# Kernel tuning notes

Measured on AMD Instinct MI355X. Metric: run time of the kernel, lower is better.

## Reference

```python
import jax, jax.numpy as jnp
import numpy as np
import math

Q_DIM = 1024
K_DIM = 1024
ATT_DIM = 1024
POS_DIM = 64
B, NQ, NK = 4, 2048, 2048
EPS = 1e-5


def _ln(x, g, b):
    m = jnp.mean(x, axis=-1, keepdims=True)
    v = jnp.var(x, axis=-1, keepdims=True)
    return (x - m) * jax.lax.rsqrt(v + EPS) * g + b


def _sinpos(n, dim):
    # SinPos: exp = 2*arange(dim//2)/dim; pos = p * 10000**-exp; cat(pos, pos+pi/2); sin
    e = 2.0 * jnp.arange(dim // 2, dtype=jnp.float32) / dim      # [dim/2]
    p = jnp.arange(n, dtype=jnp.float32)[:, None]                # [n,1]
    ph = p * jnp.power(10000.0, -e)[None, :]                     # [n,dim/2]
    return jnp.sin(jnp.concatenate([ph, ph + math.pi / 2], axis=1))  # [n,dim]


def setup_inputs() -> dict:
    key = jax.random.key(0)
    ks = jax.random.split(key, 8)
    s = 0.02
    return {
        "q": jax.random.normal(ks[0], (B, NQ, Q_DIM), jnp.float32),
        "k": jax.random.normal(ks[1], (B, NK, K_DIM), jnp.float32),
        "Wq": jax.random.normal(ks[2], (Q_DIM, ATT_DIM), jnp.float32) * s,
        "bq": jnp.zeros((ATT_DIM,), jnp.float32),
        "Wk": jax.random.normal(ks[3], (K_DIM, ATT_DIM), jnp.float32) * s,
        "bk": jnp.zeros((ATT_DIM,), jnp.float32),
        "Wv": jax.random.normal(ks[4], (K_DIM, ATT_DIM), jnp.float32) * s,
        "bv": jnp.zeros((ATT_DIM,), jnp.float32),
        "gq": jnp.ones((ATT_DIM,), jnp.float32), "betaq": jnp.zeros((ATT_DIM,), jnp.float32),
        "gk": jnp.ones((ATT_DIM,), jnp.float32), "betak": jnp.zeros((ATT_DIM,), jnp.float32),
        "gv": jnp.ones((ATT_DIM,), jnp.float32), "betav": jnp.zeros((ATT_DIM,), jnp.float32),
        "Wp": jax.random.normal(ks[5], (POS_DIM, POS_DIM), jnp.float32) * s,
        "bp": jnp.zeros((POS_DIM,), jnp.float32),
    }


def reference(q, k, Wq, bq, Wk, bk, Wv, bv, gq, betaq, gk, betak, gv, betav, Wp, bp):
    qn = _ln(q @ Wq + bq, gq, betaq)          # [B,NQ,D]
    vn = _ln(k @ Wv + bv, gv, betav)          # [B,NK,D]
    kn = _ln(k @ Wk + bk, gk, betak)          # [B,NK,D]
    pos = _sinpos(NK, POS_DIM)                # [NK,P]

    # attention 1: Q=qn, K=kn, V=pos
    s1 = jnp.einsum('bnd,bjd->bnj', qn, kn) * (1.0 / math.sqrt(ATT_DIM))
    a1 = jax.nn.softmax(s1, axis=-1)          # [B,NQ,NK]
    x = jnp.einsum('bnj,jp->bnp', a1, pos)    # [B,NQ,P]

    # pos_net (Linear)
    x = x @ Wp + bp                           # [B,NQ,P]

    # attention 2: Q=x, K=pos, V=vn
    s2 = jnp.einsum('bnp,jp->bnj', x, pos) * (1.0 / math.sqrt(POS_DIM))
    a2 = jax.nn.softmax(s2, axis=-1)          # [B,NQ,NK]
    out = jnp.einsum('bnj,bjd->bnd', a2, vn)  # [B,NQ,D]

    att = jnp.stack([a1, a2], axis=1)         # [B,2,NQ,NK] == torch.cat over head dim
    return out, att
```

## Files before the change

### kernel.cpp

```cpp
#include <hip/hip_runtime.h>
#include <math.h>
#include <stdint.h>


typedef _Float16 f16;
typedef _Float16 f16x4 __attribute__((ext_vector_type(4)));
typedef _Float16 f16x8 __attribute__((ext_vector_type(8)));
typedef float f32x4 __attribute__((ext_vector_type(4)));

static constexpr int CB  = 4;
static constexpr int CNQ = 2048;
static constexpr int CNK = 2048;
static constexpr int CD  = 1024;
static constexpr int CP  = 64;

static __device__ __forceinline__ void async16(const f16* gp, f16* lp) {
  __builtin_amdgcn_global_load_lds(
      (const __attribute__((address_space(1))) void*)(uintptr_t)gp,
      (__attribute__((address_space(3))) void*)(uint32_t)(uintptr_t)lp,
      16, 0, 0);
}

__global__ __launch_bounds__(256) void prep_kernel(
    const float* __restrict__ q, const float* __restrict__ k,
    const float* __restrict__ Wq, const float* __restrict__ Wk,
    const float* __restrict__ Wv,
    f16* __restrict__ q16, f16* __restrict__ k16,
    f16* __restrict__ WqT, f16* __restrict__ WkvT,
    f16* __restrict__ posb, f16* __restrict__ posTb) {
  const int b = blockIdx.x;
  if (b < 512) {
    int tid = b * 256 + threadIdx.x;
    int p = tid >> 11;
    int j = tid & (CNK - 1);
    int i = p & 31;
    float ph = (float)j * powf(10000.0f, -(float)i * (1.0f / 32.0f));
    float v = (p < 32) ? sinf(ph) : cosf(ph);
    posb[j * CP + p]   = (f16)v;
    posTb[p * CNK + j] = (f16)v;
  } else if (b < 512 + 16384) {
    const int NF4 = CB * CNQ * CD / 4;
    int tid = (b - 512) * 256 + threadIdx.x;
    const float* src = (tid < NF4) ? q : k;
    f16* dst = (tid < NF4) ? q16 : k16;
    int i = (tid < NF4) ? tid : tid - NF4;
    float4 v = reinterpret_cast<const float4*>(src)[i];
    f16x4 o = {(f16)v.x, (f16)v.y, (f16)v.z, (f16)v.w};
    reinterpret_cast<f16x4*>(dst)[i] = o;
  } else {
    __shared__ float t[64][65];
    const int idx = b - 16896;
    const int z = idx >> 8;
    const int rem = idx & 255;
    const float* W = (z == 0) ? Wq : (z == 1) ? Wk : Wv;
    f16* WT = (z == 0) ? WqT : (z == 1) ? WkvT : WkvT + 1024 * 1024;
    int k0 = (rem & 15) * 64, n0 = (rem >> 4) * 64;
    int tx = threadIdx.x & 63, ty = threadIdx.x >> 6;
#pragma unroll
    for (int i = 0; i < 16; i++)
      t[ty + 4 * i][tx] = W[(size_t)(k0 + ty + 4 * i) * CD + n0 + tx];
    __syncthreads();
#pragma unroll
    for (int i = 0; i < 16; i++)
      WT[(size_t)(n0 + 4 * i + ty) * CD + k0 + tx] = (f16)t[tx][ty + 4 * i];
  }
}

__global__ __launch_bounds__(256) void transpose_kernel(const f16* __restrict__ in,
                                                        f16* __restrict__ out,
                                                        int ldi) {
  __shared__ f16 t[64][65];
  int n0 = blockIdx.x * 64, d0 = blockIdx.y * 64;
  size_t ibase = (size_t)blockIdx.z * CNK * ldi;
  size_t obase = (size_t)blockIdx.z * CNK * CD;
  int tx = threadIdx.x & 63, ty = threadIdx.x >> 6;
#pragma unroll
  for (int i = 0; i < 16; i++)
    t[ty + 4 * i][tx] = in[ibase + (size_t)(n0 + ty + 4 * i) * ldi + d0 + tx];
  __syncthreads();
#pragma unroll
  for (int i = 0; i < 16; i++)
    out[obase + (size_t)(d0 + ty + 4 * i) * CNK + n0 + tx] = t[tx][ty + 4 * i];
}

template <int BM, int BN>
__device__ __forceinline__ void gemm_core3(
    const f16* __restrict__ Ab, const f16* __restrict__ Bb,
    int lda, int ldb, int K, int m0, int n0, f16* sm,
    f32x4 (&acc)[BM / 32][BN / 64]) {
  constexpr int FM = BM / 32, FN = BN / 64;
  constexpr int TI = (BM + BN) / 64;
  constexpr int bufsz = (BM + BN) * 64;
  const int tid = threadIdx.x;
  const int lane = tid & 63, wid = tid >> 6;
  const int wr = wid >> 2, wc = wid & 3;
  const int lrow = lane & 15, kg = lane >> 4;

  auto stage = [&](int i, int kt, int buf) {
    const int s = i * 512 + tid;
    const int row = s >> 3;
    const int cb = (s & 7) << 4;
    const int scb = cb ^ ((row & 7) << 4);
    const f16* src = (i < BM / 64)
        ? Ab + (size_t)(m0 + row) * lda + kt * 64 + (scb >> 1)
        : Bb + (size_t)(n0 + row - BM) * ldb + kt * 64 + (scb >> 1);
    async16(src, &sm[buf * bufsz + s * 8]);
  };

  const int NT = K >> 6;
#pragma unroll
  for (int i = 0; i < TI; i++) stage(i, 0, 0);
#pragma unroll
  for (int i = 0; i < TI; i++) stage(i, 1, 1);

  for (int t = 0; t < NT; ++t) {
    if (t + 2 < NT) {
      const int b2 = (t + 2) % 3;
#pragma unroll
      for (int i = 0; i < TI; i++) stage(i, t + 2, b2);
      asm volatile("s_waitcnt vmcnt(12)" ::: "memory");
    } else if (t + 2 == NT) {
      asm volatile("s_waitcnt vmcnt(6)" ::: "memory");
    } else {
      asm volatile("s_waitcnt vmcnt(0)" ::: "memory");
    }
    __builtin_amdgcn_s_barrier();

    const f16* smA = sm + (t % 3) * bufsz;
    const f16* smB = smA + BM * 64;
#pragma unroll
    for (int kk = 0; kk < 2; ++kk) {
      const int Cb = kk * 64 + kg * 16;
      f16x8 af[FM], bf[FN];
#pragma unroll
      for (int m = 0; m < FM; ++m) {
        const int ar = wr * (BM / 2) + m * 16 + lrow;
        af[m] = *reinterpret_cast<const f16x8*>(
            &smA[ar * 64 + ((Cb ^ ((ar & 7) << 4)) >> 1)]);
      }
#pragma unroll
      for (int n = 0; n < FN; ++n) {
        const int br = wc * (BN / 4) + n * 16 + lrow;
        bf[n] = *reinterpret_cast<const f16x8*>(
            &smB[br * 64 + ((Cb ^ ((br & 7) << 4)) >> 1)]);
      }
      __builtin_amdgcn_s_barrier();
      __builtin_amdgcn_s_setprio(1);
#pragma unroll
      for (int m = 0; m < FM; ++m)
#pragma unroll
        for (int n = 0; n < FN; ++n)
          acc[m][n] = __builtin_amdgcn_mfma_f32_16x16x32_f16(af[m], bf[n], acc[m][n], 0, 0, 0);
      __builtin_amdgcn_s_setprio(0);
      __builtin_amdgcn_s_barrier();
    }
  }
}

template <int BM, int BN>
__device__ __forceinline__ void epi_f16(
    f32x4 (&acc)[BM / 32][BN / 64], f16* sm, f16* Cp, int ldc, int m0, int n0) {
  const int tid = threadIdx.x, lane = tid & 63, wid = tid >> 6;
  const int wr = wid >> 2, wc = wid & 3;
  const int rbase = wr * (BM / 2) + (lane >> 4) * 4;
  const int cbase = wc * (BN / 4) + (lane & 15);
  __syncthreads();
#pragma unroll
  for (int mg = 0; mg < BM / 32; mg++)
#pragma unroll
    for (int n = 0; n < BN / 64; n++)
#pragma unroll
      for (int r = 0; r < 4; r++)
        sm[(rbase + mg * 16 + r) * BN + cbase + n * 16] = (f16)acc[mg][n][r];
  __syncthreads();
  constexpr int CH = BM * BN / (512 * 8);
#pragma unroll
  for (int c = 0; c < CH; c++) {
    const int idx = c * 512 + tid;
    const int row = idx / (BN / 8);
    const int cole = (idx % (BN / 8)) * 8;
    f16x8 v = *reinterpret_cast<const f16x8*>(&sm[row * BN + cole]);
    *reinterpret_cast<f16x8*>(Cp + (size_t)(m0 + row) * ldc + n0 + cole) = v;
  }
}

template <int BM, int BN>
__device__ __forceinline__ void epi_exp(
    f32x4 (&acc)[BM / 32][BN / 64], f16* sm, float* psum, f16* Cp, int ldc,
    int m0, int n0, float scale, float* PSrow) {
  constexpr int SL = BN / 8;
  const int tid = threadIdx.x, lane = tid & 63, wid = tid >> 6;
  const int wr = wid >> 2, wc = wid & 3;
  const int rbase = wr * (BM / 2) + (lane >> 4) * 4;
  const int cbase = wc * (BN / 4) + (lane & 15);
  __syncthreads();
#pragma unroll
  for (int mg = 0; mg < BM / 32; mg++)
#pragma unroll
    for (int n = 0; n < BN / 64; n++)
#pragma unroll
      for (int r = 0; r < 4; r++)
        sm[(rbase + mg * 16 + r) * BN + cbase + n * 16] =
            (f16)__expf(acc[mg][n][r] * scale);
  __syncthreads();
  constexpr int CH = BM * BN / (512 * 8);
#pragma unroll
  for (int c = 0; c < CH; c++) {
    const int idx = c * 512 + tid;
    const int row = idx / SL;
    const int cole = (idx % SL) * 8;
    f16x8 v = *reinterpret_cast<const f16x8*>(&sm[row * BN + cole]);
    *reinterpret_cast<f16x8*>(Cp + (size_t)(m0 + row) * ldc + n0 + cole) = v;
    float p = 0.f;
#pragma unroll
    for (int j = 0; j < 8; j++) p += (float)v[j];
#pragma unroll
    for (int o = 1; o < SL; o <<= 1) p += __shfl_xor(p, o);
    if ((lane & (SL - 1)) == 0) psum[row] = p;
  }
  __syncthreads();
  if (tid < BM) PSrow[tid] = psum[tid];
}

template <int BM, int BN>
__device__ __forceinline__ void epi_f32(
    f32x4 (&acc)[BM / 32][BN / 64], f16* smh, float* Cp, int ldc, int m0, int n0) {
  float* st = (float*)smh;
  const int tid = threadIdx.x, lane = tid & 63, wid = tid >> 6;
  const int wr = wid >> 2, wc = wid & 3;
  const int cbase = wc * (BN / 4) + (lane & 15);
#pragma unroll
  for (int half = 0; half < 2; half++) {
    __syncthreads();
    if (wr == half) {
#pragma unroll
      for (int mg = 0; mg < BM / 32; mg++)
#pragma unroll
        for (int r = 0; r < 4; r++) {
          const int rloc = (lane >> 4) * 4 + mg * 16 + r;
#pragma unroll
          for (int n = 0; n < BN / 64; n++)
            st[rloc * BN + cbase + n * 16] = acc[mg][n][r];
        }
    }
    __syncthreads();
    constexpr int CH = (BM / 2) * BN / (512 * 4);
#pragma unroll
    for (int c = 0; c < CH; c++) {
      const int idx = c * 512 + tid;
      const int row = idx / (BN / 4);
      const int cole = (idx % (BN / 4)) * 4;
      float4 v = *reinterpret_cast<const float4*>(&st[row * BN + cole]);
      *reinterpret_cast<float4*>(
          Cp + (size_t)(m0 + half * (BM / 2) + row) * ldc + n0 + cole) = v;
    }
  }
}

__global__ __launch_bounds__(512) void gemmIn_kernel(
    const f16* __restrict__ q16, const f16* __restrict__ WqT, f16* __restrict__ tmpq,
    const f16* __restrict__ k16, const f16* __restrict__ WkvT, f16* __restrict__ tmp2) {
  __shared__ __attribute__((aligned(16))) f16 sm[3 * (256 + 128) * 64];
  const int b = blockIdx.x;
  const int swz = (b & 7) * 96 + (b >> 3);
  const f16 *A, *B;
  f16* C;
  int ldc, m0, n0;
  if (swz < 256) {
    const int by = swz >> 5, bx = swz & 31;
    A = q16; B = WqT; C = tmpq; ldc = 1024; m0 = bx * 256; n0 = by * 128;
  } else {
    const int idx = swz - 256;
    const int by = idx >> 5, bx = idx & 31;
    A = k16; B = WkvT; C = tmp2; ldc = 2048; m0 = bx * 256; n0 = by * 128;
  }
  f32x4 acc[8][2] = {};
  gemm_core3<256, 128>(A, B, 1024, 1024, 1024, m0, n0, sm, acc);
  epi_f16<256, 128>(acc, sm, C, ldc, m0, n0);
}

__global__ __launch_bounds__(512) void gemmS1_kernel(
    const f16* __restrict__ qn, const f16* __restrict__ kn,
    f16* __restrict__ e1, float* __restrict__ PS) {
  __shared__ __attribute__((aligned(16))) f16 sm[3 * (256 + 128) * 64];
  __shared__ float psum[256];
  const int b = blockIdx.x;
  const int swz = (b & 7) * 64 + (b >> 3);
  const int bz = swz >> 7;
  const int rem = swz & 127;
  const int by = rem >> 3, bx = rem & 7;
  const int m0 = bx * 256, n0 = by * 128;
  const f16* Ab = qn + (size_t)bz * 2048 * 1024;
  const f16* Bb = kn + (size_t)bz * 2048 * 2048;
  f16* Cp = e1 + (size_t)bz * 2048 * 2048;
  f32x4 acc[8][2] = {};
  gemm_core3<256, 128>(Ab, Bb, 1024, 2048, 1024, m0, n0, sm, acc);
  epi_exp<256, 128>(acc, sm, psum, Cp, 2048, m0, n0, 0.03125f,
                    PS + (size_t)by * 8192 + bz * 2048 + m0);
}

__global__ __launch_bounds__(512) void gemmOut_kernel(
    const f16* __restrict__ e2, const f16* __restrict__ vnT, float* __restrict__ out) {
  __shared__ __attribute__((aligned(16))) f16 sm[3 * (256 + 128) * 64];
  const int b = blockIdx.x;
  const int swz = (b & 7) * 32 + (b >> 3);
  const int bz = swz >> 6;
  const int rem = swz & 63;
  const int by = rem >> 3, bx = rem & 7;
  const int m0 = bx * 256, n0 = by * 128;
  const f16* Ab = e2 + (size_t)bz * 2048 * 2048;
  const f16* Bb = vnT + (size_t)bz * 1024 * 2048;
  float* Cp = out + (size_t)bz * 2048 * 1024;
  f32x4 acc[8][2] = {};
  gemm_core3<256, 128>(Ab, Bb, 2048, 2048, 2048, m0, n0, sm, acc);
  epi_f32<256, 128>(acc, sm, Cp, 1024, m0, n0);
}

__global__ __launch_bounds__(256) void ln3_kernel(
    f16* __restrict__ tmpq, f16* __restrict__ tmp2,
    const float* __restrict__ bq, const float* __restrict__ gq, const float* __restrict__ beq,
    const float* __restrict__ bk, const float* __restrict__ gk, const float* __restrict__ bek,
    const float* __restrict__ bv, const float* __restrict__ gv, const float* __restrict__ bev) {
  __shared__ float rs_[4], rq_[4];
  const int z = blockIdx.y;
  f16* rp;
  const float *bias, *g, *beta;
  if (z == 0)      { rp = tmpq + (size_t)blockIdx.x * 1024;        bias = bq; g = gq; beta = beq; }
  else if (z == 1) { rp = tmp2 + (size_t)blockIdx.x * 2048;        bias = bk; g = gk; beta = bek; }
  else             { rp = tmp2 + (size_t)blockIdx.x * 2048 + 1024; bias = bv; g = gv; beta = bev; }
  const int t = threadIdx.x;
  f16x4 v = *reinterpret_cast<const f16x4*>(rp + t * 4);
  float y[4], s = 0.f, q = 0.f;
#pragma unroll
  for (int j = 0; j < 4; j++) {
    y[j] = (float)v[j] + bias[t * 4 + j];
    s += y[j]; q += y[j] * y[j];
  }
#pragma unroll
  for (int o = 32; o; o >>= 1) { s += __shfl_xor(s, o); q += __shfl_xor(q, o); }
  if ((t & 63) == 0) { rs_[t >> 6] = s; rq_[t >> 6] = q; }
  __syncthreads();
  s = rs_[0] + rs_[1] + rs_[2] + rs_[3];
  q = rq_[0] + rq_[1] + rq_[2] + rq_[3];
  const float mean = s * (1.0f / CD);
  const float rstd = rsqrtf(q * (1.0f / CD) - mean * mean + 1e-5f);
  f16x4 o;
#pragma unroll
  for (int j = 0; j < 4; j++) {
    int c = t * 4 + j;
    o[j] = (f16)((y[j] - mean) * rstd * g[c] + beta[c]);
  }
  *reinterpret_cast<f16x4*>(rp + t * 4) = o;
}

__global__ __launch_bounds__(256) void xgemm_kernel(
    const f16* __restrict__ e1, const f16* __restrict__ posTb,
    const float* __restrict__ PS, float* __restrict__ xw, float* __restrict__ att) {
  constexpr int BM = 64, BN = 64;
  __shared__ __attribute__((aligned(16))) f16 As[BM * 32];
  __shared__ __attribute__((aligned(16))) f16 Bs[BN * 32];
  __shared__ float invs[BM];
  const int tid = threadIdx.x;
  const int lane = tid & 63;
  const int wave = tid >> 6;
  const int wr = wave >> 1, wc = wave & 1;
  const int m0 = blockIdx.x * BM;
  const int kbase = blockIdx.z * 1024;
  const int srow = lane >> 2;
  const int scol = (lane & 3) * 8;
  const int lrow = lane & 15;
  const int kg = lane >> 4;

  if (tid < BM) {
    float s = 0.f;
#pragma unroll
    for (int j = 0; j < 16; j++) s += PS[j * (CB * CNQ) + m0 + tid];
    invs[tid] = 1.0f / s;
  }

  const int bb = m0 >> 11, nloc = m0 & (CNQ - 1);
  float* attb = att + ((size_t)(bb << 1) * CNQ + nloc) * CNK + kbase;
  const int arow = tid >> 2, acol = (tid & 3) * 8;

  f32x4 acc[2][2] = {};
  for (int k0 = 0; k0 < 1024; k0 += 32) {
    __syncthreads();
#pragma unroll
    for (int i = wave; i < 8; i += 4) {
      if (i < 4)
        async16(e1 + (size_t)(m0 + i * 16 + srow) * CNK + kbase + k0 + scol, &As[i * 512]);
      else
        async16(posTb + (size_t)((i - 4) * 16 + srow) * CNK + kbase + k0 + scol,
                &Bs[(i - 4) * 512]);
    }
    __syncthreads();
    f16x8 af[2], bfr[2];
#pragma unroll
    for (int m = 0; m < 2; m++)
      af[m] = *reinterpret_cast<const f16x8*>(&As[(wr * 32 + m * 16 + lrow) * 32 + kg * 8]);
#pragma unroll
    for (int n = 0; n < 2; n++)
      bfr[n] = *reinterpret_cast<const f16x8*>(&Bs[(wc * 32 + n * 16 + lrow) * 32 + kg * 8]);
#pragma unroll
    for (int m = 0; m < 2; m++)
#pragma unroll
      for (int n = 0; n < 2; n++)
        acc[m][n] = __builtin_amdgcn_mfma_f32_16x16x32_f16(af[m], bfr[n], acc[m][n], 0, 0, 0);
    {
      const float iv = invs[arow];
      f16x8 v = *reinterpret_cast<const f16x8*>(&As[arow * 32 + acol]);
      float4 w0 = {(float)v[0] * iv, (float)v[1] * iv, (float)v[2] * iv, (float)v[3] * iv};
      float4 w1 = {(float)v[4] * iv, (float)v[5] * iv, (float)v[6] * iv, (float)v[7] * iv};
      float* ap = attb + (size_t)arow * CNK + k0 + acol;
      reinterpret_cast<float4*>(ap)[0] = w0;
      reinterpret_cast<float4*>(ap)[1] = w1;
    }
  }
  float* Cp = xw + (size_t)blockIdx.z * (CB * CNQ) * CP;
  const int crow = m0 + wr * 32 + (lane >> 4) * 4;
  const int ccol = wc * 32 + (lane & 15);
#pragma unroll
  for (int m = 0; m < 2; m++)
#pragma unroll
    for (int n = 0; n < 2; n++)
#pragma unroll
      for (int r = 0; r < 4; r++)
        Cp[(size_t)(crow + m * 16 + r) * CP + ccol + n * 16] = acc[m][n][r];
}

__global__ __launch_bounds__(128) void attn2_kernel(
    const float* __restrict__ xw, const float* __restrict__ Wp,
    const float* __restrict__ bp, const f16* __restrict__ posb,
    const float* __restrict__ PS, f16* __restrict__ e2,
    float* __restrict__ att) {
  __shared__ __attribute__((aligned(16))) f16 shm[32 * 2048 + 32 * 64];
  __shared__ float rsum[32];
  __shared__ float invs[32];
  f16* e2lds = shm;
  f16* xpb = shm + 32 * 2048;
  float* xs = (float*)shm;
  float* Wps = (float*)shm + 32 * 64;
  const int tid = threadIdx.x, l = tid & 63, w = tid >> 6;
  const int r0 = blockIdx.x * 32;
  if (tid < 32) {
    float s = 0.f;
#pragma unroll
    for (int j = 0; j < 16; j++) s += PS[j * (CB * CNQ) + r0 + tid];
    invs[tid] = 1.0f / s;
  }
  __syncthreads();
#pragma unroll
  for (int i = 0; i < 16; i++) {
    const int row = w * 16 + i;
    const size_t gi = (size_t)(r0 + row) * CP + l;
    xs[row * 64 + l] = (xw[gi] + xw[(size_t)(CB * CNQ) * CP + gi]) * invs[row];
  }
#pragma unroll
  for (int i = w; i < 64; i += 2) Wps[i * 64 + l] = Wp[i * 64 + l];
  const float bpl = bp[l];
  __syncthreads();
  const int rb = w * 16;
#pragma unroll 2
  for (int i = 0; i < 16; i++) {
    float a = bpl;
#pragma unroll 8
    for (int p = 0; p < 64; p++) a = fmaf(xs[(rb + i) * 64 + p], Wps[p * 64 + l], a);
    xpb[(rb + i) * 64 + l] = (f16)a;
  }
  __syncthreads();
  const f16x8 af0 = *reinterpret_cast<const f16x8*>(&xpb[(rb + (l & 15)) * 64 + (l >> 4) * 8]);
  const f16x8 af1 = *reinterpret_cast<const f16x8*>(&xpb[(rb + (l & 15)) * 64 + 32 + (l >> 4) * 8]);
  float rs[4] = {0.f, 0.f, 0.f, 0.f};
  for (int jt = 0; jt < CNK / 64; jt++) {
#pragma unroll
    for (int q4 = 0; q4 < 4; q4++) {
      const int j = jt * 64 + q4 * 16 + (l & 15);
      const f16* pp = posb + (size_t)j * CP + (l >> 4) * 8;
      f16x8 b0 = *reinterpret_cast<const f16x8*>(pp);
      f16x8 b1 = *reinterpret_cast<const f16x8*>(pp + 32);
      f32x4 c = {};
      c = __builtin_amdgcn_mfma_f32_16x16x32_f16(af0, b0, c, 0, 0, 0);
      c = __builtin_amdgcn_mfma_f32_16x16x32_f16(af1, b1, c, 0, 0, 0);
#pragma unroll
      for (int r = 0; r < 4; r++) {
        float ev = __expf(c[r] * 0.125f);
        rs[r] += ev;
        e2lds[(rb + (l >> 4) * 4 + r) * 2048 + j] = (f16)ev;
      }
    }
  }
#pragma unroll
  for (int r = 0; r < 4; r++) {
#pragma unroll
    for (int o = 1; o < 16; o <<= 1) rs[r] += __shfl_xor(rs[r], o);
    if ((l & 15) == 0) rsum[rb + (l >> 4) * 4 + r] = rs[r];
  }
  __syncthreads();
  const int b = r0 >> 11, nloc = r0 & (CNQ - 1);
  float* attb = att + ((size_t)((b << 1) + 1) * CNQ + nloc) * CNK;
  f16* e2b = e2 + (size_t)r0 * CNK;
  for (int row = 0; row < 32; row++) {
    const float iv = 1.0f / rsum[row];
    const f16x8 a0 = *reinterpret_cast<const f16x8*>(&e2lds[row * 2048 + tid * 16]);
    const f16x8 a1 = *reinterpret_cast<const f16x8*>(&e2lds[row * 2048 + tid * 16 + 8]);
    float4 w0 = {(float)a0[0] * iv, (float)a0[1] * iv, (float)a0[2] * iv, (float)a0[3] * iv};
    float4 w1 = {(float)a0[4] * iv, (float)a0[5] * iv, (float)a0[6] * iv, (float)a0[7] * iv};
    float4 w2 = {(float)a1[0] * iv, (float)a1[1] * iv, (float)a1[2] * iv, (float)a1[3] * iv};
    float4 w3 = {(float)a1[4] * iv, (float)a1[5] * iv, (float)a1[6] * iv, (float)a1[7] * iv};
    float* ap = attb + (size_t)row * CNK + tid * 16;
    reinterpret_cast<float4*>(ap)[0] = w0;
    reinterpret_cast<float4*>(ap)[1] = w1;
    reinterpret_cast<float4*>(ap)[2] = w2;
    reinterpret_cast<float4*>(ap)[3] = w3;
    f16x8 h0 = {(f16)w0.x, (f16)w0.y, (f16)w0.z, (f16)w0.w,
                (f16)w1.x, (f16)w1.y, (f16)w1.z, (f16)w1.w};
    f16x8 h1 = {(f16)w2.x, (f16)w2.y, (f16)w2.z, (f16)w2.w,
                (f16)w3.x, (f16)w3.y, (f16)w3.z, (f16)w3.w};
    f16* ep = e2b + (size_t)row * CNK + tid * 16;
    *reinterpret_cast<f16x8*>(ep)     = h0;
    *reinterpret_cast<f16x8*>(ep + 8) = h1;
  }
}

extern "C" void kernel_launch(void* const* d_in, const int* in_sizes, int n_in,
                              void* d_out, int out_size, void* d_ws, size_t ws_size,
                              hipStream_t stream) {
  (void)in_sizes; (void)n_in; (void)out_size; (void)ws_size;
  const float* q    = (const float*)d_in[0];
  const float* k    = (const float*)d_in[1];
  const float* Wq   = (const float*)d_in[2];
  const float* bq   = (const float*)d_in[3];
  const float* Wk   = (const float*)d_in[4];
  const float* bk   = (const float*)d_in[5];
  const float* Wv   = (const float*)d_in[6];
  const float* bv   = (const float*)d_in[7];
  const float* gq   = (const float*)d_in[8];
  const float* betaq= (const float*)d_in[9];
  const float* gk   = (const float*)d_in[10];
  const float* betak= (const float*)d_in[11];
  const float* gv   = (const float*)d_in[12];
  const float* betav= (const float*)d_in[13];
  const float* Wp   = (const float*)d_in[14];
  const float* bp   = (const float*)d_in[15];

  float* out = (float*)d_out;
  float* att = out + (size_t)CB * CNQ * CD;
  char* ws = (char*)d_ws;
  const size_t MB = 1ull << 20;

  f16* q16   = (f16*)(ws);
  f16* k16   = (f16*)(ws + 16 * MB);
  f16* e1    = (f16*)(ws);
  f16* e2    = (f16*)(ws);
  f16* WqT   = (f16*)(ws + 32 * MB);
  f16* WkvT  = (f16*)(ws + 34 * MB);
  f16* posb  = (f16*)(ws + 38 * MB);
  f16* posTb = (f16*)(ws + 38 * MB + 256 * 1024);
  float* xw  = (float*)(ws + 38 * MB + 512 * 1024);
  float* PS  = (float*)(ws + 42 * MB + 512 * 1024);
  f16* tmpq  = (f16*)(ws + 43 * MB);
  f16* tmp2  = (f16*)(ws + 59 * MB);
  f16* vnT   = (f16*)(ws + 91 * MB);
  f16* qn = tmpq;
  f16* kn = tmp2;
  f16* vn = tmp2 + 1024;

  prep_kernel<<<512 + 16384 + 768, 256, 0, stream>>>(
      q, k, Wq, Wk, Wv, q16, k16, WqT, WkvT, posb, posTb);

  gemmIn_kernel<<<768, 512, 0, stream>>>(q16, WqT, tmpq, k16, WkvT, tmp2);
  ln3_kernel<<<dim3(CB * CNQ, 3), 256, 0, stream>>>(
      tmpq, tmp2, bq, gq, betaq, bk, gk, betak, bv, gv, betav);
  transpose_kernel<<<dim3(CNK / 64, CD / 64, CB), 256, 0, stream>>>(vn, vnT, 2048);

  gemmS1_kernel<<<512, 512, 0, stream>>>(qn, kn, e1, PS);

  xgemm_kernel<<<dim3(CB * CNQ / 64, 1, 2), 256, 0, stream>>>(e1, posTb, PS, xw, att);
  attn2_kernel<<<CB * CNQ / 32, 128, 0, stream>>>(xw, Wp, bp, posb, PS, e2, att);

  gemmOut_kernel<<<256, 512, 0, stream>>>(e2, vnT, out);
}
```

Before: 323.7 us.

## Retile GEMMs to double-buffered 128x256/256x256 tiles and widen attn2 blocks

```diff
diff --git a/kernel.cpp b/kernel.cpp
--- a/kernel.cpp
+++ b/kernel.cpp
@@ -84,11 +84,12 @@
 }
 
 template <int BM, int BN>
-__device__ __forceinline__ void gemm_core3(
+__device__ __forceinline__ void gemm_core(
     const f16* __restrict__ Ab, const f16* __restrict__ Bb,
     int lda, int ldb, int K, int m0, int n0, f16* sm,
-    f32x4 (&acc)[BM / 32][BN / 64]) {
-  constexpr int FM = BM / 32, FN = BN / 64;
+    f32x4 (&acc)[BM / 32][4]) {
+  constexpr int FM = BM / 32;
+  constexpr int FMC = FM / 2;
   constexpr int TI = (BM + BN) / 64;
   constexpr int bufsz = (BM + BN) * 64;
   const int tid = threadIdx.x;
@@ -107,50 +108,52 @@
     async16(src, &sm[buf * bufsz + s * 8]);
   };
 
-  const int NT = K >> 6;
+  const int NTk = K >> 6;
 #pragma unroll
   for (int i = 0; i < TI; i++) stage(i, 0, 0);
-#pragma unroll
-  for (int i = 0; i < TI; i++) stage(i, 1, 1);
-
-  for (int t = 0; t < NT; ++t) {
-    if (t + 2 < NT) {
-      const int b2 = (t + 2) % 3;
-#pragma unroll
-      for (int i = 0; i < TI; i++) stage(i, t + 2, b2);
-      asm volatile("s_waitcnt vmcnt(12)" ::: "memory");
-    } else if (t + 2 == NT) {
-      asm volatile("s_waitcnt vmcnt(6)" ::: "memory");
+
+  for (int t = 0; t < NTk; ++t) {
+    const int cur = t & 1;
+    if (t + 1 < NTk) {
+#pragma unroll
+      for (int i = 0; i < TI; i++) stage(i, t + 1, cur ^ 1);
+      if constexpr (TI == 8) asm volatile("s_waitcnt vmcnt(8)" ::: "memory");
+      else                   asm volatile("s_waitcnt vmcnt(6)" ::: "memory");
     } else {
       asm volatile("s_waitcnt vmcnt(0)" ::: "memory");
     }
     __builtin_amdgcn_s_barrier();
 
-    const f16* smA = sm + (t % 3) * bufsz;
+    const f16* smA = sm + cur * bufsz;
     const f16* smB = smA + BM * 64;
-#pragma unroll
-    for (int kk = 0; kk < 2; ++kk) {
+    f16x8 bf[2][4];
+#pragma unroll
+    for (int p = 0; p < 4; ++p) {
+      const int kk = p >> 1, mh = p & 1;
       const int Cb = kk * 64 + kg * 16;
-      f16x8 af[FM], bf[FN];
-#pragma unroll
-      for (int m = 0; m < FM; ++m) {
-        const int ar = wr * (BM / 2) + m * 16 + lrow;
+      f16x8 af[FMC];
+#pragma unroll
+      for (int m = 0; m < FMC; ++m) {
+        const int ar = wr * (BM / 2) + mh * (FMC * 16) + m * 16 + lrow;
         af[m] = *reinterpret_cast<const f16x8*>(
             &smA[ar * 64 + ((Cb ^ ((ar & 7) << 4)) >> 1)]);
       }
-#pragma unroll
-      for (int n = 0; n < FN; ++n) {
-        const int br = wc * (BN / 4) + n * 16 + lrow;
-        bf[n] = *reinterpret_cast<const f16x8*>(
-            &smB[br * 64 + ((Cb ^ ((br & 7) << 4)) >> 1)]);
+      if (mh == 0) {
+#pragma unroll
+        for (int n = 0; n < 4; ++n) {
+          const int br = wc * 64 + n * 16 + lrow;
+          bf[kk][n] = *reinterpret_cast<const f16x8*>(
+              &smB[br * 64 + ((Cb ^ ((br & 7) << 4)) >> 1)]);
+        }
       }
       __builtin_amdgcn_s_barrier();
       __builtin_amdgcn_s_setprio(1);
 #pragma unroll
-      for (int m = 0; m < FM; ++m)
-#pragma unroll
-        for (int n = 0; n < FN; ++n)
-          acc[m][n] = __builtin_amdgcn_mfma_f32_16x16x32_f16(af[m], bf[n], acc[m][n], 0, 0, 0);
+      for (int m = 0; m < FMC; ++m)
+#pragma unroll
+        for (int n = 0; n < 4; ++n)
+          acc[mh * FMC + m][n] = __builtin_amdgcn_mfma_f32_16x16x32_f16(
+              af[m], bf[kk][n], acc[mh * FMC + m][n], 0, 0, 0);
       __builtin_amdgcn_s_setprio(0);
       __builtin_amdgcn_s_barrier();
     }
@@ -159,16 +162,16 @@
 
 template <int BM, int BN>
 __device__ __forceinline__ void epi_f16(
-    f32x4 (&acc)[BM / 32][BN / 64], f16* sm, f16* Cp, int ldc, int m0, int n0) {
+    f32x4 (&acc)[BM / 32][4], f16* sm, f16* Cp, int ldc, int m0, int n0) {
   const int tid = threadIdx.x, lane = tid & 63, wid = tid >> 6;
   const int wr = wid >> 2, wc = wid & 3;
   const int rbase = wr * (BM / 2) + (lane >> 4) * 4;
-  const int cbase = wc * (BN / 4) + (lane & 15);
+  const int cbase = wc * 64 + (lane & 15);
   __syncthreads();
 #pragma unroll
   for (int mg = 0; mg < BM / 32; mg++)
 #pragma unroll
-    for (int n = 0; n < BN / 64; n++)
+    for (int n = 0; n < 4; n++)
 #pragma unroll
       for (int r = 0; r < 4; r++)
         sm[(rbase + mg * 16 + r) * BN + cbase + n * 16] = (f16)acc[mg][n][r];
@@ -186,18 +189,18 @@
 
 template <int BM, int BN>
 __device__ __forceinline__ void epi_exp(
-    f32x4 (&acc)[BM / 32][BN / 64], f16* sm, float* psum, f16* Cp, int ldc,
+    f32x4 (&acc)[BM / 32][4], f16* sm, float* psum, f16* Cp, int ldc,
     int m0, int n0, float scale, float* PSrow) {
   constexpr int SL = BN / 8;
   const int tid = threadIdx.x, lane = tid & 63, wid = tid >> 6;
   const int wr = wid >> 2, wc = wid & 3;
   const int rbase = wr * (BM / 2) + (lane >> 4) * 4;
-  const int cbase = wc * (BN / 4) + (lane & 15);
+  const int cbase = wc * 64 + (lane & 15);
   __syncthreads();
 #pragma unroll
   for (int mg = 0; mg < BM / 32; mg++)
 #pragma unroll
-    for (int n = 0; n < BN / 64; n++)
+    for (int n = 0; n < 4; n++)
 #pragma unroll
       for (int r = 0; r < 4; r++)
         sm[(rbase + mg * 16 + r) * BN + cbase + n * 16] =
@@ -224,11 +227,11 @@
 
 template <int BM, int BN>
 __device__ __forceinline__ void epi_f32(
-    f32x4 (&acc)[BM / 32][BN / 64], f16* smh, float* Cp, int ldc, int m0, int n0) {
+    f32x4 (&acc)[BM / 32][4], f16* smh, float* Cp, int ldc, int m0, int n0) {
   float* st = (float*)smh;
   const int tid = threadIdx.x, lane = tid & 63, wid = tid >> 6;
   const int wr = wid >> 2, wc = wid & 3;
-  const int cbase = wc * (BN / 4) + (lane & 15);
+  const int cbase = wc * 64 + (lane & 15);
 #pragma unroll
   for (int half = 0; half < 2; half++) {
     __syncthreads();
@@ -239,7 +242,7 @@
         for (int r = 0; r < 4; r++) {
           const int rloc = (lane >> 4) * 4 + mg * 16 + r;
 #pragma unroll
-          for (int n = 0; n < BN / 64; n++)
+          for (int n = 0; n < 4; n++)
             st[rloc * BN + cbase + n * 16] = acc[mg][n][r];
         }
     }
@@ -260,60 +263,60 @@
 __global__ __launch_bounds__(512) void gemmIn_kernel(
     const f16* __restrict__ q16, const f16* __restrict__ WqT, f16* __restrict__ tmpq,
     const f16* __restrict__ k16, const f16* __restrict__ WkvT, f16* __restrict__ tmp2) {
-  __shared__ __attribute__((aligned(16))) f16 sm[3 * (256 + 128) * 64];
+  __shared__ __attribute__((aligned(16))) f16 sm[2 * (128 + 256) * 64];
   const int b = blockIdx.x;
   const int swz = (b & 7) * 96 + (b >> 3);
   const f16 *A, *B;
   f16* C;
   int ldc, m0, n0;
   if (swz < 256) {
-    const int by = swz >> 5, bx = swz & 31;
-    A = q16; B = WqT; C = tmpq; ldc = 1024; m0 = bx * 256; n0 = by * 128;
+    const int bx = swz & 63, by = swz >> 6;
+    A = q16; B = WqT; C = tmpq; ldc = 1024; m0 = bx * 128; n0 = by * 256;
   } else {
     const int idx = swz - 256;
-    const int by = idx >> 5, bx = idx & 31;
-    A = k16; B = WkvT; C = tmp2; ldc = 2048; m0 = bx * 256; n0 = by * 128;
-  }
-  f32x4 acc[8][2] = {};
-  gemm_core3<256, 128>(A, B, 1024, 1024, 1024, m0, n0, sm, acc);
-  epi_f16<256, 128>(acc, sm, C, ldc, m0, n0);
+    const int bx = idx & 63, by = idx >> 6;
+    A = k16; B = WkvT; C = tmp2; ldc = 2048; m0 = bx * 128; n0 = by * 256;
+  }
+  f32x4 acc[4][4] = {};
+  gemm_core<128, 256>(A, B, 1024, 1024, 1024, m0, n0, sm, acc);
+  epi_f16<128, 256>(acc, sm, C, ldc, m0, n0);
 }
 
 __global__ __launch_bounds__(512) void gemmS1_kernel(
     const f16* __restrict__ qn, const f16* __restrict__ kn,
     f16* __restrict__ e1, float* __restrict__ PS) {
-  __shared__ __attribute__((aligned(16))) f16 sm[3 * (256 + 128) * 64];
+  __shared__ __attribute__((aligned(16))) f16 sm[2 * (256 + 256) * 64];
   __shared__ float psum[256];
-  const int b = blockIdx.x;
-  const int swz = (b & 7) * 64 + (b >> 3);
-  const int bz = swz >> 7;
-  const int rem = swz & 127;
-  const int by = rem >> 3, bx = rem & 7;
-  const int m0 = bx * 256, n0 = by * 128;
-  const f16* Ab = qn + (size_t)bz * 2048 * 1024;
-  const f16* Bb = kn + (size_t)bz * 2048 * 2048;
-  f16* Cp = e1 + (size_t)bz * 2048 * 2048;
-  f32x4 acc[8][2] = {};
-  gemm_core3<256, 128>(Ab, Bb, 1024, 2048, 1024, m0, n0, sm, acc);
-  epi_exp<256, 128>(acc, sm, psum, Cp, 2048, m0, n0, 0.03125f,
-                    PS + (size_t)by * 8192 + bz * 2048 + m0);
-}
-
-__global__ __launch_bounds__(512) void gemmOut_kernel(
-    const f16* __restrict__ e2, const f16* __restrict__ vnT, float* __restrict__ out) {
-  __shared__ __attribute__((aligned(16))) f16 sm[3 * (256 + 128) * 64];
   const int b = blockIdx.x;
   const int swz = (b & 7) * 32 + (b >> 3);
   const int bz = swz >> 6;
   const int rem = swz & 63;
-  const int by = rem >> 3, bx = rem & 7;
-  const int m0 = bx * 256, n0 = by * 128;
+  const int bx = rem & 7, by = rem >> 3;
+  const int m0 = bx * 256, n0 = by * 256;
+  const f16* Ab = qn + (size_t)bz * 2048 * 1024;
+  const f16* Bb = kn + (size_t)bz * 2048 * 2048;
+  f16* Cp = e1 + (size_t)bz * 2048 * 2048;
+  f32x4 acc[8][4] = {};
+  gemm_core<256, 256>(Ab, Bb, 1024, 2048, 1024, m0, n0, sm, acc);
+  epi_exp<256, 256>(acc, sm, psum, Cp, 2048, m0, n0, 0.03125f,
+                    PS + (size_t)by * (CB * CNQ) + bz * 2048 + m0);
+}
+
+__global__ __launch_bounds__(512) void gemmOut_kernel(
+    const f16* __restrict__ e2, const f16* __restrict__ vnT, float* __restrict__ out) {
+  __shared__ __attribute__((aligned(16))) f16 sm[2 * (128 + 256) * 64];
+  const int b = blockIdx.x;
+  const int swz = (b & 7) * 32 + (b >> 3);
+  const int bz = swz >> 6;
+  const int rem = swz & 63;
+  const int bx = rem & 15, by = rem >> 4;
+  const int m0 = bx * 128, n0 = by * 256;
   const f16* Ab = e2 + (size_t)bz * 2048 * 2048;
   const f16* Bb = vnT + (size_t)bz * 1024 * 2048;
   float* Cp = out + (size_t)bz * 2048 * 1024;
-  f32x4 acc[8][2] = {};
-  gemm_core3<256, 128>(Ab, Bb, 2048, 2048, 2048, m0, n0, sm, acc);
-  epi_f32<256, 128>(acc, sm, Cp, 1024, m0, n0);
+  f32x4 acc[4][4] = {};
+  gemm_core<128, 256>(Ab, Bb, 2048, 2048, 2048, m0, n0, sm, acc);
+  epi_f32<128, 256>(acc, sm, Cp, 1024, m0, n0);
 }
 
 __global__ __launch_bounds__(256) void ln3_kernel(
@@ -374,7 +377,7 @@
   if (tid < BM) {
     float s = 0.f;
 #pragma unroll
-    for (int j = 0; j < 16; j++) s += PS[j * (CB * CNQ) + m0 + tid];
+    for (int j = 0; j < 8; j++) s += PS[j * (CB * CNQ) + m0 + tid];
     invs[tid] = 1.0f / s;
   }
 
@@ -428,13 +431,13 @@
         Cp[(size_t)(crow + m * 16 + r) * CP + ccol + n * 16] = acc[m][n][r];
 }
 
-__global__ __launch_bounds__(128) void attn2_kernel(
+__global__ __launch_bounds__(256) void attn2_kernel(
     const float* __restrict__ xw, const float* __restrict__ Wp,
     const float* __restrict__ bp, const f16* __restrict__ posb,
     const float* __restrict__ PS, f16* __restrict__ e2,
     float* __restrict__ att) {
   __shared__ __attribute__((aligned(16))) f16 shm[32 * 2048 + 32 * 64];
-  __shared__ float rsum[32];
+  __shared__ float rsum2[2][32];
   __shared__ float invs[32];
   f16* e2lds = shm;
   f16* xpb = shm + 32 * 2048;
@@ -445,33 +448,37 @@
   if (tid < 32) {
     float s = 0.f;
 #pragma unroll
-    for (int j = 0; j < 16; j++) s += PS[j * (CB * CNQ) + r0 + tid];
+    for (int j = 0; j < 8; j++) s += PS[j * (CB * CNQ) + r0 + tid];
     invs[tid] = 1.0f / s;
   }
   __syncthreads();
-#pragma unroll
-  for (int i = 0; i < 16; i++) {
-    const int row = w * 16 + i;
-    const size_t gi = (size_t)(r0 + row) * CP + l;
-    xs[row * 64 + l] = (xw[gi] + xw[(size_t)(CB * CNQ) * CP + gi]) * invs[row];
-  }
-#pragma unroll
-  for (int i = w; i < 64; i += 2) Wps[i * 64 + l] = Wp[i * 64 + l];
+  if (w < 2) {
+#pragma unroll
+    for (int i = 0; i < 16; i++) {
+      const int row = w * 16 + i;
+      const size_t gi = (size_t)(r0 + row) * CP + l;
+      xs[row * 64 + l] = (xw[gi] + xw[(size_t)(CB * CNQ) * CP + gi]) * invs[row];
+    }
+#pragma unroll
+    for (int i = w; i < 64; i += 2) Wps[i * 64 + l] = Wp[i * 64 + l];
+  }
   const float bpl = bp[l];
   __syncthreads();
-  const int rb = w * 16;
+  const int rb = (w & 1) * 16, jh = w >> 1;
+  if (w < 2) {
 #pragma unroll 2
-  for (int i = 0; i < 16; i++) {
-    float a = bpl;
+    for (int i = 0; i < 16; i++) {
+      float a = bpl;
 #pragma unroll 8
-    for (int p = 0; p < 64; p++) a = fmaf(xs[(rb + i) * 64 + p], Wps[p * 64 + l], a);
-    xpb[(rb + i) * 64 + l] = (f16)a;
+      for (int p = 0; p < 64; p++) a = fmaf(xs[(w * 16 + i) * 64 + p], Wps[p * 64 + l], a);
+      xpb[(w * 16 + i) * 64 + l] = (f16)a;
+    }
   }
   __syncthreads();
   const f16x8 af0 = *reinterpret_cast<const f16x8*>(&xpb[(rb + (l & 15)) * 64 + (l >> 4) * 8]);
   const f16x8 af1 = *reinterpret_cast<const f16x8*>(&xpb[(rb + (l & 15)) * 64 + 32 + (l >> 4) * 8]);
   float rs[4] = {0.f, 0.f, 0.f, 0.f};
-  for (int jt = 0; jt < CNK / 64; jt++) {
+  for (int jt = jh * 16; jt < jh * 16 + 16; jt++) {
 #pragma unroll
     for (int q4 = 0; q4 < 4; q4++) {
       const int j = jt * 64 + q4 * 16 + (l & 15);
@@ -493,21 +500,23 @@
   for (int r = 0; r < 4; r++) {
 #pragma unroll
     for (int o = 1; o < 16; o <<= 1) rs[r] += __shfl_xor(rs[r], o);
-    if ((l & 15) == 0) rsum[rb + (l >> 4) * 4 + r] = rs[r];
+    if ((l & 15) == 0) rsum2[jh][rb + (l >> 4) * 4 + r] = rs[r];
   }
   __syncthreads();
   const int b = r0 >> 11, nloc = r0 & (CNQ - 1);
   float* attb = att + ((size_t)((b << 1) + 1) * CNQ + nloc) * CNK;
   f16* e2b = e2 + (size_t)r0 * CNK;
-  for (int row = 0; row < 32; row++) {
-    const float iv = 1.0f / rsum[row];
-    const f16x8 a0 = *reinterpret_cast<const f16x8*>(&e2lds[row * 2048 + tid * 16]);
-    const f16x8 a1 = *reinterpret_cast<const f16x8*>(&e2lds[row * 2048 + tid * 16 + 8]);
+  for (int it = 0; it < 16; it++) {
+    const int row = it * 2 + (tid >> 7);
+    const int col = (tid & 127) * 16;
+    const float iv = 1.0f / (rsum2[0][row] + rsum2[1][row]);
+    const f16x8 a0 = *reinterpret_cast<const f16x8*>(&e2lds[row * 2048 + col]);
+    const f16x8 a1 = *reinterpret_cast<const f16x8*>(&e2lds[row * 2048 + col + 8]);
     float4 w0 = {(float)a0[0] * iv, (float)a0[1] * iv, (float)a0[2] * iv, (float)a0[3] * iv};
     float4 w1 = {(float)a0[4] * iv, (float)a0[5] * iv, (float)a0[6] * iv, (float)a0[7] * iv};
     float4 w2 = {(float)a1[0] * iv, (float)a1[1] * iv, (float)a1[2] * iv, (float)a1[3] * iv};
     float4 w3 = {(float)a1[4] * iv, (float)a1[5] * iv, (float)a1[6] * iv, (float)a1[7] * iv};
-    float* ap = attb + (size_t)row * CNK + tid * 16;
+    float* ap = attb + (size_t)row * CNK + col;
     reinterpret_cast<float4*>(ap)[0] = w0;
     reinterpret_cast<float4*>(ap)[1] = w1;
     reinterpret_cast<float4*>(ap)[2] = w2;
@@ -516,7 +525,7 @@
                 (f16)w1.x, (f16)w1.y, (f16)w1.z, (f16)w1.w};
     f16x8 h1 = {(f16)w2.x, (f16)w2.y, (f16)w2.z, (f16)w2.w,
                 (f16)w3.x, (f16)w3.y, (f16)w3.z, (f16)w3.w};
-    f16* ep = e2b + (size_t)row * CNK + tid * 16;
+    f16* ep = e2b + (size_t)row * CNK + col;
     *reinterpret_cast<f16x8*>(ep)     = h0;
     *reinterpret_cast<f16x8*>(ep + 8) = h1;
   }
@@ -573,10 +582,10 @@
       tmpq, tmp2, bq, gq, betaq, bk, gk, betak, bv, gv, betav);
   transpose_kernel<<<dim3(CNK / 64, CD / 64, CB), 256, 0, stream>>>(vn, vnT, 2048);
 
-  gemmS1_kernel<<<512, 512, 0, stream>>>(qn, kn, e1, PS);
+  gemmS1_kernel<<<256, 512, 0, stream>>>(qn, kn, e1, PS);
 
   xgemm_kernel<<<dim3(CB * CNQ / 64, 1, 2), 256, 0, stream>>>(e1, posTb, PS, xw, att);
-  attn2_kernel<<<CB * CNQ / 32, 128, 0, stream>>>(xw, Wp, bp, posb, PS, e2, att);
+  attn2_kernel<<<CB * CNQ / 32, 256, 0, stream>>>(xw, Wp, bp, posb, PS, e2, att);
 
   gemmOut_kernel<<<256, 512, 0, stream>>>(e2, vnT, out);
 }
```

Result: faster. 296.8 us (-8.3%).
